# Kernel optimization log

Measured on AMD Instinct MI355X. Metric: run time of the kernel, lower is better.

The kernel has to match this reference:

```python
import jax, jax.numpy as jnp
import numpy as np

DEPTH = 11


def setup_inputs() -> dict:
    key = jax.random.key(0)
    k1, k2, k3 = jax.random.split(key, 3)
    B, S, D = 4, 4096, 768
    n_nodes = 2 * DEPTH - 1  # 21
    return {
        "inputs": jax.random.normal(k1, (B, S, D), dtype=jnp.float32),
        "weights_in": jax.random.normal(k2, (n_nodes, D), dtype=jnp.float32),
        "weights_out": jax.random.normal(k3, (n_nodes, D), dtype=jnp.float32),
    }


def _fff_forward(inputs, weights_in, weights_out, depth=DEPTH):
    B, S, _ = inputs.shape
    n_nodes = weights_in.shape[0]
    max_index = n_nodes - 1

    # Dot product of every token with every tree-node weight once: (B,S,n_nodes).
    # Mathematically identical to gathering weights_in[sel] per level and taking
    # a per-token dot product, but avoids materializing (B,S,D) gathers per step.
    all_logits = jnp.einsum('bsd,nd->bsn', inputs, weights_in)

    def step(prev_idx, _):
        sel = jnp.clip(prev_idx, 0, max_index)
        logits = jnp.take_along_axis(all_logits, sel[..., None], axis=-1)[..., 0]  # (B,S)
        new_idx = jnp.clip(2 * sel + 1 + (logits > 0).astype(sel.dtype), 0, max_index)
        return new_idx, (logits, new_idx)

    idx0 = jnp.zeros((B, S), dtype=jnp.int32)
    _, (logits_seq, idx_seq) = jax.lax.scan(step, idx0, None, length=depth - 1)

    # Level 0 has logit=0 (gelu(0)=0 -> zero contribution) and node index 0.
    logits = jnp.concatenate(
        [jnp.zeros((1, B, S), all_logits.dtype), logits_seq], axis=0)  # (depth,B,S)
    node_idx = jnp.concatenate([idx0[None], idx_seq], axis=0)          # (depth,B,S)

    act = jax.nn.gelu(logits, approximate=False)  # exact erf GELU = torch.nn.GELU

    # out[b,s,:] = sum_d act[d,b,s] * weights_out[node_idx[d,b,s], :]
    # Scatter the 11 per-level activations into per-node coefficients (B,S,21),
    # then one small dense matmul against the 21x768 output table.
    onehot = jax.nn.one_hot(node_idx, n_nodes, dtype=act.dtype)  # (depth,B,S,n)
    coeff = jnp.einsum('dbs,dbsn->bsn', act, onehot)             # (B,S,n)
    return jnp.einsum('bsn,nd->bsd', coeff, weights_out)         # (B,S,D)


def reference(inputs, weights_in, weights_out):
    return _fff_forward(inputs, weights_in, weights_out)
```

## Files before the change

kernel.cpp:

```cpp
#include <hip/hip_runtime.h>
#include <math.h>


#define D 768
#define NF4 (D / 4)
#define NN 21
#define TPB 1024
#define NBLK 256
#define NWAVES (NBLK * (TPB / 64))

__device__ __forceinline__ float gelu_exact(float v) {
  return 0.5f * v * (1.0f + erff(v * 0.70710678118654752440f));
}

template <int CTRL>
__device__ __forceinline__ float dppadd(float v) {
  int m = __builtin_amdgcn_update_dpp(0, __float_as_int(v), CTRL, 0xF, 0xF, true);
  return v + __int_as_float(m);
}

__device__ __forceinline__ float wave_red(float v) {
  v = dppadd<0x140>(v);
  v = dppadd<0x141>(v);
  v = dppadd<0x4E>(v);
  v = dppadd<0xB1>(v);
  v += __shfl_xor(v, 16);
  v += __shfl_xor(v, 32);
  return v;
}

__device__ __forceinline__ float dot12(float4 a0, float4 a1, float4 a2,
                                       float4 w0, float4 w1, float4 w2) {
  float s = a0.x * w0.x;
  s = fmaf(a0.y, w0.y, s); s = fmaf(a0.z, w0.z, s); s = fmaf(a0.w, w0.w, s);
  s = fmaf(a1.x, w1.x, s); s = fmaf(a1.y, w1.y, s); s = fmaf(a1.z, w1.z, s);
  s = fmaf(a1.w, w1.w, s); s = fmaf(a2.x, w2.x, s); s = fmaf(a2.y, w2.y, s);
  s = fmaf(a2.z, w2.z, s); s = fmaf(a2.w, w2.w, s);
  return s;
}

__device__ __forceinline__ void accrow(const float* __restrict__ row, int lane,
                                       float g, float4& a0, float4& a1,
                                       float4& a2) {
  const float4* r = (const float4*)row;
  float4 w0 = r[lane], w1 = r[lane + 64], w2 = r[lane + 128];
  a0.x = fmaf(g, w0.x, a0.x); a0.y = fmaf(g, w0.y, a0.y);
  a0.z = fmaf(g, w0.z, a0.z); a0.w = fmaf(g, w0.w, a0.w);
  a1.x = fmaf(g, w1.x, a1.x); a1.y = fmaf(g, w1.y, a1.y);
  a1.z = fmaf(g, w1.z, a1.z); a1.w = fmaf(g, w1.w, a1.w);
  a2.x = fmaf(g, w2.x, a2.x); a2.y = fmaf(g, w2.y, a2.y);
  a2.z = fmaf(g, w2.z, a2.z); a2.w = fmaf(g, w2.w, a2.w);
}

__device__ __forceinline__ void token_out(const float (&r)[NN],
                                          const float* __restrict__ s_wo,
                                          int lane, float* __restrict__ outp) {
  float l0 = r[0];
  int b0 = l0 > 0.0f;
  float l1 = b0 ? r[2] : r[1];
  int b1 = l1 > 0.0f;
  float l2 = b0 ? (b1 ? r[6] : r[5]) : (b1 ? r[4] : r[3]);
  int b2 = l2 > 0.0f;
  float m0 = b2 ? r[8] : r[7];
  float m1 = b2 ? r[10] : r[9];
  float m2 = b2 ? r[12] : r[11];
  float m3 = b2 ? r[14] : r[13];
  float l3 = b0 ? (b1 ? m3 : m2) : (b1 ? m1 : m0);
  int b3 = l3 > 0.0f;
  int i4 = (b0 << 3) | (b1 << 2) | (b2 << 1) | b3;
  float l4 = r[15];
  l4 = (i4 >= 1) ? r[16] : l4;
  l4 = (i4 >= 2) ? r[17] : l4;
  l4 = (i4 >= 3) ? r[18] : l4;
  l4 = (i4 >= 4) ? r[19] : l4;
  l4 = (i4 >= 5) ? r[20] : l4;

  int u1 = 1 + b0;
  int u2 = 3 + 2 * b0 + b1;
  int u3 = 7 + 4 * b0 + 2 * b1 + b2;
  int u4 = 15 + (i4 < 5 ? i4 : 5);

  float g1 = gelu_exact(l0);
  float g2 = gelu_exact(l1);
  float g3 = gelu_exact(l2);
  float g4 = gelu_exact(l3);
  float g5 = gelu_exact(l4) + 5.0f * gelu_exact(r[20]);

  float4 a0 = {0.f, 0.f, 0.f, 0.f}, a1 = a0, a2 = a0;
  accrow(s_wo + u1 * D, lane, g1, a0, a1, a2);
  accrow(s_wo + u2 * D, lane, g2, a0, a1, a2);
  accrow(s_wo + u3 * D, lane, g3, a0, a1, a2);
  accrow(s_wo + u4 * D, lane, g4, a0, a1, a2);
  accrow(s_wo + (NN - 1) * D, lane, g5, a0, a1, a2);

  float4* op = (float4*)outp;
  op[lane] = a0;
  op[lane + 64] = a1;
  op[lane + 128] = a2;
}

__global__ __launch_bounds__(TPB, 1) void fff_kernel(
    const float* __restrict__ x, const float* __restrict__ wi,
    const float* __restrict__ wo, float* __restrict__ out, int ntok) {
  __shared__ __align__(16) float s_wi[NN * D];
  __shared__ __align__(16) float s_wo[NN * D];

  const int tid = threadIdx.x;
  {
    const float4* a = (const float4*)wi;
    const float4* b = (const float4*)wo;
    float4* sa = (float4*)s_wi;
    float4* sb = (float4*)s_wo;
    for (int i = tid; i < NN * NF4; i += TPB) {
      sa[i] = a[i];
      sb[i] = b[i];
    }
  }
  __syncthreads();

  const int lane = tid & 63;
  const int wid = (blockIdx.x << 4) | (tid >> 6);
  const float4* swi4 = (const float4*)s_wi;

  for (int tA = wid; tA < ntok; tA += 2 * NWAVES) {
    const int tB = tA + NWAVES;
    const bool hasB = tB < ntok;
    const float4* xa = (const float4*)(x + (size_t)tA * D);
    float4 xa0 = xa[lane], xa1 = xa[lane + 64], xa2 = xa[lane + 128];
    const float4* xb = (const float4*)(x + (size_t)(hasB ? tB : tA) * D);
    float4 xb0 = xb[lane], xb1 = xb[lane + 64], xb2 = xb[lane + 128];

    float rA[NN], rB[NN];
#pragma unroll
    for (int n = 0; n < NN; ++n) {
      float4 w0 = swi4[n * NF4 + lane];
      float4 w1 = swi4[n * NF4 + lane + 64];
      float4 w2 = swi4[n * NF4 + lane + 128];
      rA[n] = dot12(xa0, xa1, xa2, w0, w1, w2);
      rB[n] = dot12(xb0, xb1, xb2, w0, w1, w2);
    }
#pragma unroll
    for (int n = 0; n < NN; ++n) {
      rA[n] = wave_red(rA[n]);
      rB[n] = wave_red(rB[n]);
    }

    token_out(rA, s_wo, lane, out + (size_t)tA * D);
    if (hasB) token_out(rB, s_wo, lane, out + (size_t)tB * D);
  }
}

extern "C" void kernel_launch(void* const* d_in, const int* in_sizes, int n_in,
                              void* d_out, int out_size, void* d_ws,
                              size_t ws_size, hipStream_t stream) {
  const float* x = (const float*)d_in[0];
  const float* wi = (const float*)d_in[1];
  const float* wo = (const float*)d_in[2];
  float* out = (float*)d_out;
  const int ntok = in_sizes[0] / D;
  fff_kernel<<<NBLK, TPB, 0, stream>>>(x, wi, wo, out, ntok);
}
```

Baseline: 151.6 us.

## Read output weights from global memory and halve block size for occupancy

Drops the shared-memory copy of weights_out so each block only stages weights_in (about 64KB instead of 129KB). Output rows are now read from global memory through a wave-uniform, readfirstlane-scalarised index and served by L2/L1. The launch changes to 512 blocks of 512 threads with launch_bounds allowing 4 blocks per CU, which should raise occupancy and cut the per-block staging cost. The trade-off is that weights_out reads now go through the cache hierarchy instead of LDS, and the extra occupancy could raise register pressure.

Measured after the change: 156.9 us. 3.5% more time.

```diff
diff --git a/kernel.cpp b/kernel.cpp
--- a/kernel.cpp
+++ b/kernel.cpp
@@ -5,8 +5,8 @@
 #define D 768
 #define NF4 (D / 4)
 #define NN 21
-#define TPB 1024
-#define NBLK 256
+#define TPB 512
+#define NBLK 512
 #define NWAVES (NBLK * (TPB / 64))
 
 __device__ __forceinline__ float gelu_exact(float v) {
@@ -39,10 +39,11 @@
   return s;
 }
 
-__device__ __forceinline__ void accrow(const float* __restrict__ row, int lane,
-                                       float g, float4& a0, float4& a1,
-                                       float4& a2) {
-  const float4* r = (const float4*)row;
+__device__ __forceinline__ void accrow_g(const float* __restrict__ wo, int u,
+                                         int lane, float g, float4& a0,
+                                         float4& a1, float4& a2) {
+  const float4* r =
+      (const float4*)(wo + (size_t)__builtin_amdgcn_readfirstlane(u) * D);
   float4 w0 = r[lane], w1 = r[lane + 64], w2 = r[lane + 128];
   a0.x = fmaf(g, w0.x, a0.x); a0.y = fmaf(g, w0.y, a0.y);
   a0.z = fmaf(g, w0.z, a0.z); a0.w = fmaf(g, w0.w, a0.w);
@@ -53,7 +54,7 @@
 }
 
 __device__ __forceinline__ void token_out(const float (&r)[NN],
-                                          const float* __restrict__ s_wo,
+                                          const float* __restrict__ wo,
                                           int lane, float* __restrict__ outp) {
   float l0 = r[0];
   int b0 = l0 > 0.0f;
@@ -87,11 +88,11 @@
   float g5 = gelu_exact(l4) + 5.0f * gelu_exact(r[20]);
 
   float4 a0 = {0.f, 0.f, 0.f, 0.f}, a1 = a0, a2 = a0;
-  accrow(s_wo + u1 * D, lane, g1, a0, a1, a2);
-  accrow(s_wo + u2 * D, lane, g2, a0, a1, a2);
-  accrow(s_wo + u3 * D, lane, g3, a0, a1, a2);
-  accrow(s_wo + u4 * D, lane, g4, a0, a1, a2);
-  accrow(s_wo + (NN - 1) * D, lane, g5, a0, a1, a2);
+  accrow_g(wo, u1, lane, g1, a0, a1, a2);
+  accrow_g(wo, u2, lane, g2, a0, a1, a2);
+  accrow_g(wo, u3, lane, g3, a0, a1, a2);
+  accrow_g(wo, u4, lane, g4, a0, a1, a2);
+  accrow_g(wo, NN - 1, lane, g5, a0, a1, a2);
 
   float4* op = (float4*)outp;
   op[lane] = a0;
@@ -99,27 +100,21 @@
   op[lane + 128] = a2;
 }
 
-__global__ __launch_bounds__(TPB, 1) void fff_kernel(
+__global__ __launch_bounds__(TPB, 4) void fff_kernel(
     const float* __restrict__ x, const float* __restrict__ wi,
     const float* __restrict__ wo, float* __restrict__ out, int ntok) {
   __shared__ __align__(16) float s_wi[NN * D];
-  __shared__ __align__(16) float s_wo[NN * D];
 
   const int tid = threadIdx.x;
   {
     const float4* a = (const float4*)wi;
-    const float4* b = (const float4*)wo;
     float4* sa = (float4*)s_wi;
-    float4* sb = (float4*)s_wo;
-    for (int i = tid; i < NN * NF4; i += TPB) {
-      sa[i] = a[i];
-      sb[i] = b[i];
-    }
+    for (int i = tid; i < NN * NF4; i += TPB) sa[i] = a[i];
   }
   __syncthreads();
 
   const int lane = tid & 63;
-  const int wid = (blockIdx.x << 4) | (tid >> 6);
+  const int wid = (blockIdx.x << 3) | (tid >> 6);
   const float4* swi4 = (const float4*)s_wi;
 
   for (int tA = wid; tA < ntok; tA += 2 * NWAVES) {
@@ -145,8 +140,8 @@
       rB[n] = wave_red(rB[n]);
     }
 
-    token_out(rA, s_wo, lane, out + (size_t)tA * D);
-    if (hasB) token_out(rB, s_wo, lane, out + (size_t)tB * D);
+    token_out(rA, wo, lane, out + (size_t)tA * D);
+    if (hasB) token_out(rB, wo, lane, out + (size_t)tB * D);
   }
 }
 
```
